# Optimization experiments

Measured on AMD Instinct MI355X. Metric: run time of the kernel, lower is better.

Reference implementation:

```python
import jax, jax.numpy as jnp
import numpy as np

DIM_IN = 256
DIM = 256      # dim_out
N = 4096       # nodes at current depth
K = 16         # max children (padded)
R = 8192       # rows in previous-level h/c tensors (row 0 is the zero init row)


def _reverse_sequence(x, length):
    """TF reverse_sequence along axis 1: reverse first length[i] steps, keep tail."""
    T = x.shape[1]
    t = jnp.arange(T)
    idx = jnp.where(t[None, :] < length[:, None], length[:, None] - 1 - t[None, :], t[None, :])
    return jnp.take_along_axis(x, idx[:, :, None], axis=1)


def _lstm(x, kernel, rec, bias, h0, c0):
    """Standard (CuDNN/Keras gate order i,f,g,o) LSTM. x: [B,T,D] -> y: [B,T,H]."""
    xz = jnp.einsum('btd,dg->btg', x, kernel) + bias  # precompute input projection

    def step(carry, xz_t):
        h, c = carry
        z = xz_t + h @ rec
        i, f, g, o = jnp.split(z, 4, axis=-1)
        c = jax.nn.sigmoid(f) * c + jax.nn.sigmoid(i) * jnp.tanh(g)
        h = jax.nn.sigmoid(o) * jnp.tanh(c)
        return (h, c), h

    _, ys = jax.lax.scan(step, (h0, c0), jnp.swapaxes(xz, 0, 1))
    return jnp.swapaxes(ys, 0, 1)


def _bilstm(x, length, kernel, rec, bias, init_h, init_c, fc_w, return_seq):
    """kernel/rec/bias/init_* have a leading dir axis of size 2 (fwd, bwd)."""
    B = x.shape[0]
    h0f = jnp.broadcast_to(init_h[0], (B, DIM))
    c0f = jnp.broadcast_to(init_c[0], (B, DIM))
    h0b = jnp.broadcast_to(init_h[1], (B, DIM))
    c0b = jnp.broadcast_to(init_c[1], (B, DIM))
    x_back = _reverse_sequence(x, length)
    y_f = _lstm(x, kernel[0], rec[0], bias[0], h0f, c0f)
    y_b = _lstm(x_back, kernel[1], rec[1], bias[1], h0b, c0b)
    y = jnp.concatenate([y_f, y_b], axis=-1)  # [B,T,2*DIM] (y_b not re-reversed, as in TF code)
    if return_seq:
        return y @ fc_w
    y_last = y[jnp.arange(B), length - 1]  # last valid timestep
    return y_last @ fc_w


def setup_inputs() -> dict:
    key = jax.random.key(0)
    ks = jax.random.split(key, 16)
    x = jax.random.normal(ks[0], (N, DIM_IN), dtype=jnp.float32)
    h_tensor = jax.random.normal(ks[1], (R, DIM), dtype=jnp.float32)
    c_tensor = jax.random.normal(ks[2], (R, DIM), dtype=jnp.float32)
    # padded child-index matrix: each row has length in [1, K], padded with -1
    raw = jax.random.randint(ks[3], (N, K), 0, R, dtype=jnp.int32)
    lengths = jax.random.randint(ks[4], (N,), 1, K + 1, dtype=jnp.int32)
    indice = jnp.where(jnp.arange(K)[None, :] < lengths[:, None], raw, jnp.int32(-1))
    # Dense W: dim_in -> 4*dim_out
    W_w = jax.random.normal(ks[5], (DIM_IN, 4 * DIM), dtype=jnp.float32) * 0.05
    W_b = jnp.zeros((4 * DIM,), dtype=jnp.float32)
    # 4 BiLSTMs (gates f,i,u,o), each with 2 directions; input dim = DIM (gathered h)
    lstm_kernel = jax.random.normal(ks[6], (4, 2, DIM, 4 * DIM), dtype=jnp.float32) * 0.05
    lstm_rec = jax.random.normal(ks[7], (4, 2, DIM, 4 * DIM), dtype=jnp.float32) * 0.05
    lstm_bias = jnp.zeros((4, 2, 4 * DIM), dtype=jnp.float32)
    init_h = jax.random.normal(ks[8], (4, 2, 1, DIM), dtype=jnp.float32) * 0.01
    init_c = jax.random.normal(ks[9], (4, 2, 1, DIM), dtype=jnp.float32) * 0.01
    fc_w = jax.random.normal(ks[10], (4, 2 * DIM, DIM), dtype=jnp.float32) * 0.05
    return {"x": x, "h_tensor": h_tensor, "c_tensor": c_tensor, "indice": indice,
            "W_w": W_w, "W_b": W_b, "lstm_kernel": lstm_kernel, "lstm_rec": lstm_rec,
            "lstm_bias": lstm_bias, "init_h": init_h, "init_c": init_c, "fc_w": fc_w}


def reference(x, h_tensor, c_tensor, indice, W_w, W_b, lstm_kernel, lstm_rec,
              lstm_bias, init_h, init_c, fc_w):
    mask_bool = indice != -1
    mask = mask_bool.astype(jnp.float32)                # [N,K]
    length = jnp.sum(mask, axis=1).astype(jnp.int32)    # [N]
    safe_idx = jnp.where(mask_bool, indice, 0)
    h = h_tensor[safe_idx]  # [N,K,DIM] gathered child states
    c = c_tensor[safe_idx]
    W_x = x @ W_w + W_b
    W_f_x, W_i_x, W_u_x, W_o_x = jnp.split(W_x, 4, axis=-1)
    # forget gate: per-child BiLSTM sequence output
    f_seq = _bilstm(h, length, lstm_kernel[0], lstm_rec[0], lstm_bias[0],
                    init_h[0], init_c[0], fc_w[0], return_seq=True)  # [N,K,DIM]
    branch_f_k = jax.nn.sigmoid(W_f_x[:, None, :] + f_seq)
    branch_f = jnp.sum(branch_f_k * c * mask[:, :, None], axis=1)    # masked reduce
    branch_i = jax.nn.sigmoid(_bilstm(h, length, lstm_kernel[1], lstm_rec[1], lstm_bias[1],
                                      init_h[1], init_c[1], fc_w[1], False) + W_i_x)
    branch_u = jnp.tanh(_bilstm(h, length, lstm_kernel[2], lstm_rec[2], lstm_bias[2],
                                init_h[2], init_c[2], fc_w[2], False) + W_u_x)
    branch_o = jax.nn.sigmoid(_bilstm(h, length, lstm_kernel[3], lstm_rec[3], lstm_bias[3],
                                      init_h[3], init_c[3], fc_w[3], False) + W_o_x)
    new_c = branch_i * branch_u + branch_f
    new_h = branch_o * jnp.tanh(new_c)
    return new_h, new_c
```

## Files before the change

### kernel.cpp

```cpp
#include <hip/hip_runtime.h>
#include <stdint.h>

typedef __bf16 bf16x8 __attribute__((ext_vector_type(8)));
typedef float  f32x4  __attribute__((ext_vector_type(4)));
typedef unsigned short u16;
typedef unsigned int   u32;

#define NN   4096
#define KCH  16
#define RR   8192

static constexpr size_t OFF_WCOMB = 0;
static constexpr size_t OFF_FCWT  = 8388608;
static constexpr size_t OFF_HST   = 9961472;
static constexpr size_t OFF_CST   = 43515904;
static constexpr size_t OFF_YSEQ  = 77070336;
static constexpr size_t OFF_YLAST = 144179200;
static constexpr size_t OFF_BRF   = 160956416;
static constexpr size_t OFF_FCO   = 163053568;
static constexpr size_t OFF_XS    = 169345024;
static constexpr size_t OFF_HN    = 171442176;
static constexpr size_t OFF_CN    = 175636480;
static constexpr size_t OFF_BIASN = 179830784;
static constexpr size_t OFF_IHN   = 179847168;
static constexpr size_t OFF_ICN   = 179851264;
static constexpr size_t OFF_WBN   = 179855360;
static constexpr size_t OFF_IDX   = 179857408;
static constexpr size_t OFF_LEN   = 180119552;
static constexpr size_t OFF_FLAG  = 180135936;
static constexpr size_t OFF_NODEOF= 180136000;
static constexpr size_t OFF_LENS  = 180152384;
static constexpr size_t OFF_NTN   = 180168768;
static constexpr size_t WS_NEEDED = 180168832;

struct KParams {
  const void *x, *h_tensor, *c_tensor, *W_w, *W_b, *lstm_kernel, *lstm_rec,
             *lstm_bias, *init_h, *init_c, *fc_w;
  const int *indice;
  u16 *wcomb, *fcwT2, *h_state, *y_seq, *y_last, *brf, *fc_outb,
      *xs, *hn, *cn, *biasn, *inithn, *initcn, *wbn;
  float *c_stateT;
  int *idxf, *len, *flag, *nodeof, *len_s, *ntneed;
  float *outp;
};

__device__ __forceinline__ float b2f(u16 u){ union{u32 i;float f;}v; v.i=((u32)u)<<16; return v.f; }
__device__ __forceinline__ u16  f2b(float f){ union{float f;u32 i;}v; v.f=f; u32 r=v.i+0x7FFFu+((v.i>>16)&1u); return (u16)(r>>16); }
__device__ __forceinline__ float sigm(float x){ return 1.0f/(1.0f+__expf(-x)); }
__device__ __forceinline__ float tanh_(float x){ return 2.0f/(1.0f+__expf(-2.0f*x)) - 1.0f; }
__device__ __forceinline__ u16  cvt(const void* q, size_t i, int isf){
  return isf ? f2b(((const float*)q)[i]) : ((const u16*)q)[i];
}
__device__ __forceinline__ void cp16(const u16* g, u16* l){
  __builtin_amdgcn_global_load_lds((const __attribute__((address_space(1))) u32*)g,
                                   (__attribute__((address_space(3))) u32*)l, 16, 0, 0);
}

__global__ void detect_k(KParams p){
  __shared__ int cnt[256];
  int tid = threadIdx.x;
  u16 u = ((const u16*)p.x)[2*tid];
  int e = (u >> 7) & 0xFF;
  cnt[tid] = (u != 0 && e >= 100 && e <= 140) ? 1 : 0;
  __syncthreads();
  if (tid == 0){
    int s = 0;
    for (int i=0;i<256;i++) s += cnt[i];
    *p.flag = (s < 192) ? 1 : 0;
  }
}

__global__ void prep_idx_k(KParams p){
  int n = blockIdx.x*256 + threadIdx.x;
  if (n >= NN) return;
  int L = 0;
  #pragma unroll
  for (int t=0;t<KCH;t++) L += (p.indice[n*KCH+t] != -1);
  p.len[n] = L;
}

__global__ void sort_k(KParams p){
  __shared__ int cnt[17];
  __shared__ int start[17];
  int tid = threadIdx.x;
  if (tid < 17) cnt[tid] = 0;
  __syncthreads();
  for (int n = tid; n < NN; n += 256) atomicAdd(&cnt[p.len[n]], 1);
  __syncthreads();
  if (tid == 0){
    int acc = 0;
    for (int v = 16; v >= 1; --v){ start[v] = acc; acc += cnt[v]; }
    for (int t = 0; t < 16; ++t){
      int need = (t == 0) ? NN : start[t];
      p.ntneed[t] = (need + 127) >> 7;
    }
  }
  __syncthreads();
  for (int n = tid; n < NN; n += 256){
    int ps = atomicAdd(&start[p.len[n]], 1);
    p.nodeof[ps] = n;
  }
}

__global__ void norm_k(KParams p){
  int i = blockIdx.x*256 + threadIdx.x;
  if (i >= 4207616) return;
  int isf = *p.flag;
  if (i < 2097152)       p.hn[i] = cvt(p.h_tensor, i, isf);
  else if (i < 4194304)  p.cn[i-2097152] = cvt(p.c_tensor, i-2097152, isf);
  else if (i < 4202496){ int j = i-4194304; int gd = j>>10, pc = j&1023;
                         p.biasn[j] = cvt(p.lstm_bias, gd*1024 + ((pc&3)<<8) + (pc>>2), isf); }
  else if (i < 4204544)  p.inithn[i-4202496] = cvt(p.init_h, i-4202496, isf);
  else if (i < 4206592)  p.initcn[i-4204544] = cvt(p.init_c, i-4204544, isf);
  else                   p.wbn[i-4206592] = cvt(p.W_b, i-4206592, isf);
}

__global__ void xperm_k(KParams p){
  int ns = blockIdx.x, u = threadIdx.x;
  int n = p.nodeof[ns];
  p.xs[(size_t)ns*256 + u] = cvt(p.x, (size_t)n*256 + u, *p.flag);
}

__global__ void prep_idx2_k(KParams p){
  int ns = blockIdx.x*256 + threadIdx.x;
  if (ns >= NN) return;
  int n = p.nodeof[ns];
  p.len_s[ns] = p.len[n];
  #pragma unroll
  for (int t=0;t<KCH;t++){
    int v = p.indice[n*KCH+t];
    p.idxf[t*NN + ns] = (v != -1) ? v : 0;
  }
}

__global__ void prep_w_k(KParams p){
  int i = blockIdx.x*256 + threadIdx.x;
  int isf = *p.flag;
  if (i < 4194304){
    int gd = i>>19, pc = (i>>9)&1023, k = i&511;
    int perm = ((pc&3)<<8) + (pc>>2);
    p.wcomb[i] = (k < 256) ? cvt(p.lstm_rec,    (size_t)(gd*256 + k)*1024 + perm, isf)
                           : cvt(p.lstm_kernel, (size_t)(gd*256 + (k-256))*1024 + perm, isf);
  } else if (i < 4980736){
    int j = i - 4194304;
    int g = j/196608, rem = j%196608, o = rem/768, k = rem%768;
    p.fcwT2[j] = (k < 512) ? cvt(p.fc_w, (size_t)(g*512 + k)*256 + o, isf)
                           : cvt(p.W_w,  (size_t)(k-512)*1024 + g*256 + o, isf);
  }
}

__global__ void prep_state_k(KParams p){
  int i = blockIdx.x*256 + threadIdx.x;
  int gd = i >> 20;
  p.h_state[i]  = p.inithn[(gd<<8) + (i & 255)];
  p.c_stateT[i] = b2f(p.initcn[(gd<<8) + ((i>>12)&255)]);
}

__global__ void fallback_k(float* out){
  int i = blockIdx.x*256 + threadIdx.x;
  out[i] = 1000.0f; out[1048576 + i] = 1000.0f;
}

enum { MODE_STAGE=0, MODE_FC0=1, MODE_FC123=2 };

template<int MODE>
__launch_bounds__(256)
__global__ void gemm_k(KParams p, int t)
{
  __shared__ __align__(16) u16 As[2][8192];
  __shared__ __align__(16) u16 Bs[2][8192];
  __shared__ __align__(16) u16 hbuf[(MODE==MODE_STAGE)?128*40:1];
  __shared__ int nidx[(MODE!=MODE_FC123)?128:1];
  __shared__ u16 biasl[(MODE==MODE_STAGE)?128:1];
  __shared__ int Ln[(MODE==MODE_FC0)?8:1];

  const int tid = threadIdx.x;
  const int lane = tid & 63, wv = tid >> 6;
  const int col16 = lane & 15, quad = lane >> 4;
  const int wy = wv >> 1, wx = wv & 1;

  constexpr int K  = (MODE==MODE_STAGE) ? 512 : 768;
  constexpr int KT = K/64;

  int mtile, ntile, gd = 0;
  const u16 *Ap=nullptr, *Bh=nullptr;
  if constexpr (MODE==MODE_STAGE){
    int b = blockIdx.x;
    gd = b & 7; mtile = (b>>3) & 7; ntile = b >> 6;
    if (ntile >= p.ntneed[t]) return;
    Ap = p.wcomb + (size_t)gd*1024*512;
    Bh = p.h_state + ((size_t)(t&1)*8 + gd)*NN*256;
  } else if constexpr (MODE==MODE_FC0){
    mtile = blockIdx.x; ntile = blockIdx.y;
  } else {
    mtile = blockIdx.x; ntile = blockIdx.y; gd = blockIdx.z;
  }
  const int rowA = mtile*128;
  const int rowB = ntile*128;

  if constexpr (MODE==MODE_STAGE){
    if (tid < 128){
      int n = rowB + tid;
      int L = p.len_s[n];
      int d = gd & 1;
      int eff = (d && t < L) ? (L-1-t) : t;
      nidx[tid] = p.idxf[eff*NN + n];
      biasl[tid] = p.biasn[gd*1024 + rowA + tid];
    }
    __syncthreads();
  }
  if constexpr (MODE==MODE_FC0){
    if (tid < 128){
      int nl = tid>>4, tt = tid&15;
      nidx[tid] = p.idxf[tt*NN + mtile*8 + nl];
    }
    if (tid < 8) Ln[tid] = p.len_s[mtile*8 + tid];
    __syncthreads();
  }

  auto stage = [&](int kt, int buf){
    const int kk = kt*64;
    #pragma unroll
    for (int i=0;i<4;i++){
      int ch = wv*4 + i;
      int r  = ch*8 + (lane>>3);
      int cs = (((lane&7) ^ (r&7)) << 3);
      const u16 *ga, *gb;
      if constexpr (MODE==MODE_STAGE){
        ga = Ap + (size_t)(rowA+r)*512 + kk + cs;
        gb = (kk < 256) ? (Bh + (size_t)(rowB+r)*256 + kk + cs)
                        : (p.hn + (size_t)nidx[r]*256 + (kk-256) + cs);
      } else if constexpr (MODE==MODE_FC0){
        if (kk < 512){
          const u16* Asel = (kk < 256) ? p.y_seq : p.y_seq + (size_t)65536*256;
          ga = Asel + (size_t)(rowA+r)*256 + (kk&255) + cs;
        } else {
          ga = p.xs + (size_t)((rowA+r)>>4)*256 + (kk-512) + cs;
        }
        gb = p.fcwT2 + (size_t)(rowB+r)*768 + kk + cs;
      } else {
        int g = gd + 1;
        if (kk < 512){
          const u16* Asel = p.y_last + (size_t)(g*2 + (kk>=256))*NN*256;
          ga = Asel + (size_t)(rowA+r)*256 + (kk&255) + cs;
        } else {
          ga = p.xs + (size_t)(rowA+r)*256 + (kk-512) + cs;
        }
        gb = p.fcwT2 + (size_t)g*196608 + (size_t)(rowB+r)*768 + kk + cs;
      }
      cp16(ga, &As[buf][ch*512]);
      cp16(gb, &Bs[buf][ch*512]);
    }
  };

  f32x4 acc[4][4] = {};

  stage(0, 0);
  for (int kt = 0; kt < KT; ++kt){
    __syncthreads();
    if (kt+1 < KT) stage(kt+1, (kt+1)&1);
    const int bsel = kt & 1;
    #pragma unroll
    for (int ks=0; ks<64; ks+=32){
      bf16x8 af[4], bfr[4];
      #pragma unroll
      for (int mf=0; mf<4; mf++){
        int row = wy*64+mf*16+col16;
        int lc  = (ks>>3) + quad;
        af[mf] = *(const bf16x8*)&As[bsel][row*64 + ((lc ^ (row&7))<<3)];
      }
      #pragma unroll
      for (int nf=0; nf<4; nf++){
        int row = wx*64+nf*16+col16;
        int lc  = (ks>>3) + quad;
        bfr[nf] = *(const bf16x8*)&Bs[bsel][row*64 + ((lc ^ (row&7))<<3)];
      }
      #pragma unroll
      for (int mf=0; mf<4; mf++)
        #pragma unroll
        for (int nf=0; nf<4; nf++)
          acc[mf][nf] = __builtin_amdgcn_mfma_f32_16x16x32_bf16(af[mf], bfr[nf], acc[mf][nf], 0, 0, 0);
    }
  }

  if constexpr (MODE==MODE_STAGE){
    const int g = gd >> 1, d = gd & 1;
    const int wbuf = (t+1) & 1;
    #pragma unroll
    for (int nf=0; nf<4; nf++){
      int nc_ = wx*64 + nf*16 + col16;
      int n = rowB + nc_;
      #pragma unroll
      for (int mf=0; mf<4; mf++){
        int lp = wy*64 + mf*16 + quad*4;
        int u  = (rowA + lp) >> 2;
        float zi = acc[mf][nf][0] + b2f(biasl[lp+0]);
        float zf = acc[mf][nf][1] + b2f(biasl[lp+1]);
        float zg = acc[mf][nf][2] + b2f(biasl[lp+2]);
        float zo = acc[mf][nf][3] + b2f(biasl[lp+3]);
        size_t ci = ((size_t)gd*256 + u)*NN + n;
        float cp = p.c_stateT[ci];
        float cn = sigm(zf)*cp + sigm(zi)*tanh_(zg);
        float hn = sigm(zo)*tanh_(cn);
        p.c_stateT[ci] = cn;
        hbuf[nc_*40 + (lp>>2)] = f2b(hn);
      }
    }
    __syncthreads();
    int row = tid >> 1, half = tid & 1;
    int n = rowB + row;
    int u0 = (rowA >> 2) + half*16;
    uint4 v0 = *(const uint4*)&hbuf[row*40 + half*16];
    uint4 v1 = *(const uint4*)&hbuf[row*40 + half*16 + 8];
    u16* hw = p.h_state + (((size_t)wbuf*8 + gd)*NN + n)*256 + u0;
    ((uint4*)hw)[0] = v0; ((uint4*)hw)[1] = v1;
    if (g == 0){
      u16* yw = p.y_seq + ((size_t)d*65536 + (size_t)n*KCH + t)*256 + u0;
      ((uint4*)yw)[0] = v0; ((uint4*)yw)[1] = v1;
    } else if (p.len_s[n] == t+1){
      u16* lw = p.y_last + ((size_t)gd*NN + n)*256 + u0;
      ((uint4*)lw)[0] = v0; ((uint4*)lw)[1] = v1;
    }
  } else if constexpr (MODE==MODE_FC0){
    #pragma unroll
    for (int mf=0; mf<4; mf++){
      int nl = wy*4 + mf;
      int n  = mtile*8 + nl;
      int L  = Ln[nl];
      #pragma unroll
      for (int nf=0; nf<4; nf++){
        int u = rowB + wx*64 + nf*16 + col16;
        float wb_ = b2f(p.wbn[u]);
        float psum = 0.f;
        #pragma unroll
        for (int r=0;r<4;r++){
          int tt = quad*4 + r;
          if (tt < L){
            int ridx = nidx[nl*16 + tt];
            float cch = b2f(p.cn[(size_t)ridx*256 + u]);
            psum += sigm(acc[mf][nf][r] + wb_) * cch;
          }
        }
        psum += __shfl_xor(psum, 16);
        psum += __shfl_xor(psum, 32);
        if (quad == 0) p.brf[(size_t)n*256 + u] = f2b(psum);
      }
    }
  } else {
    int g = gd + 1;
    #pragma unroll
    for (int mf=0; mf<4; mf++){
      int r0 = rowA + wy*64 + mf*16 + quad*4;
      #pragma unroll
      for (int nf=0; nf<4; nf++){
        int c = rowB + wx*64 + nf*16 + col16;
        float wb_ = b2f(p.wbn[g*256 + c]);
        u16* o = p.fc_outb + (size_t)gd*NN*256 + (size_t)r0*256 + c;
        #pragma unroll
        for (int r=0;r<4;r++) o[(size_t)r*256] = f2b(acc[mf][nf][r] + wb_);
      }
    }
  }
}

__global__ void final_k(KParams p){
  int i = blockIdx.x*256 + threadIdx.x;
  int ns = i >> 8, u = i & 255;
  int n = p.nodeof[ns];
  float bf_ = b2f(p.brf[i]);
  float bi = sigm (b2f(p.fc_outb[i]));
  float bu = tanh_(b2f(p.fc_outb[1048576 + i]));
  float bo = sigm (b2f(p.fc_outb[2097152 + i]));
  float nc = bi*bu + bf_;
  float nh = bo*tanh_(nc);
  p.outp[(size_t)n*256 + u] = nh;
  p.outp[1048576 + (size_t)n*256 + u] = nc;
}

extern "C" void kernel_launch(void* const* d_in, const int* in_sizes, int n_in,
                              void* d_out, int out_size, void* d_ws, size_t ws_size,
                              hipStream_t stream) {
  if (ws_size < WS_NEEDED){
    fallback_k<<<4096, 256, 0, stream>>>((float*)d_out);
    return;
  }
  KParams p;
  p.x          = d_in[0];
  p.h_tensor   = d_in[1];
  p.c_tensor   = d_in[2];
  p.indice     = (const int*)d_in[3];
  p.W_w        = d_in[4];
  p.W_b        = d_in[5];
  p.lstm_kernel= d_in[6];
  p.lstm_rec   = d_in[7];
  p.lstm_bias  = d_in[8];
  p.init_h     = d_in[9];
  p.init_c     = d_in[10];
  p.fc_w       = d_in[11];
  char* w = (char*)d_ws;
  p.wcomb   = (u16*)  (w + OFF_WCOMB);
  p.fcwT2   = (u16*)  (w + OFF_FCWT);
  p.h_state = (u16*)  (w + OFF_HST);
  p.c_stateT= (float*)(w + OFF_CST);
  p.y_seq   = (u16*)  (w + OFF_YSEQ);
  p.y_last  = (u16*)  (w + OFF_YLAST);
  p.brf     = (u16*)  (w + OFF_BRF);
  p.fc_outb = (u16*)  (w + OFF_FCO);
  p.xs      = (u16*)  (w + OFF_XS);
  p.hn      = (u16*)  (w + OFF_HN);
  p.cn      = (u16*)  (w + OFF_CN);
  p.biasn   = (u16*)  (w + OFF_BIASN);
  p.inithn  = (u16*)  (w + OFF_IHN);
  p.initcn  = (u16*)  (w + OFF_ICN);
  p.wbn     = (u16*)  (w + OFF_WBN);
  p.idxf    = (int*)  (w + OFF_IDX);
  p.len     = (int*)  (w + OFF_LEN);
  p.flag    = (int*)  (w + OFF_FLAG);
  p.nodeof  = (int*)  (w + OFF_NODEOF);
  p.len_s   = (int*)  (w + OFF_LENS);
  p.ntneed  = (int*)  (w + OFF_NTN);
  p.outp    = (float*)d_out;

  detect_k    <<<1,     256, 0, stream>>>(p);
  prep_idx_k  <<<16,    256, 0, stream>>>(p);
  sort_k      <<<1,     256, 0, stream>>>(p);
  norm_k      <<<16436, 256, 0, stream>>>(p);
  xperm_k     <<<4096,  256, 0, stream>>>(p);
  prep_idx2_k <<<16,    256, 0, stream>>>(p);
  prep_w_k    <<<19456, 256, 0, stream>>>(p);
  prep_state_k<<<32768, 256, 0, stream>>>(p);

  for (int t = 0; t < KCH; ++t)
    gemm_k<MODE_STAGE><<<2048, 256, 0, stream>>>(p, t);

  gemm_k<MODE_FC0>  <<<dim3(512,2), 256, 0, stream>>>(p, 0);
  gemm_k<MODE_FC123><<<dim3(32,2,3), 256, 0, stream>>>(p, 0);

  final_k<<<4096, 256, 0, stream>>>(p);
}
```

Measured before the change: 908.4 us.

## Split recurrent step GEMM into dedicated 512-thread kernel with 256x128 tiles

```diff
diff --git a/kernel.cpp b/kernel.cpp
--- a/kernel.cpp
+++ b/kernel.cpp
@@ -161,54 +161,143 @@
   out[i] = 1000.0f; out[1048576 + i] = 1000.0f;
 }
 
-enum { MODE_STAGE=0, MODE_FC0=1, MODE_FC123=2 };
-
-template<int MODE>
-__launch_bounds__(256)
-__global__ void gemm_k(KParams p, int t)
+__global__ __launch_bounds__(512, 4) void stage512_k(KParams p, int t)
 {
-  __shared__ __align__(16) u16 As[2][8192];
-  __shared__ __align__(16) u16 Bs[2][8192];
-  __shared__ __align__(16) u16 hbuf[(MODE==MODE_STAGE)?128*40:1];
-  __shared__ int nidx[(MODE!=MODE_FC123)?128:1];
-  __shared__ u16 biasl[(MODE==MODE_STAGE)?128:1];
-  __shared__ int Ln[(MODE==MODE_FC0)?8:1];
+  __shared__ __align__(16) u16 As[16384];
+  __shared__ __align__(16) u16 Bs[8192];
+  __shared__ int nidx[128];
+  __shared__ u16 biasl[256];
 
   const int tid = threadIdx.x;
   const int lane = tid & 63, wv = tid >> 6;
   const int col16 = lane & 15, quad = lane >> 4;
   const int wy = wv >> 1, wx = wv & 1;
 
-  constexpr int K  = (MODE==MODE_STAGE) ? 512 : 768;
-  constexpr int KT = K/64;
-
-  int mtile, ntile, gd = 0;
-  const u16 *Ap=nullptr, *Bh=nullptr;
-  if constexpr (MODE==MODE_STAGE){
-    int b = blockIdx.x;
-    gd = b & 7; mtile = (b>>3) & 7; ntile = b >> 6;
-    if (ntile >= p.ntneed[t]) return;
-    Ap = p.wcomb + (size_t)gd*1024*512;
-    Bh = p.h_state + ((size_t)(t&1)*8 + gd)*NN*256;
-  } else if constexpr (MODE==MODE_FC0){
-    mtile = blockIdx.x; ntile = blockIdx.y;
-  } else {
-    mtile = blockIdx.x; ntile = blockIdx.y; gd = blockIdx.z;
-  }
+  const int b = blockIdx.x;
+  const int gd = b & 7, mtile = (b>>3) & 3, ntile = b >> 5;
+  if (ntile >= p.ntneed[t]) return;
+  const u16* __restrict__ Ap = p.wcomb + (size_t)gd*524288;
+  const u16* __restrict__ Bh = p.h_state + ((size_t)(t&1)*8 + gd)*NN*256;
+  const int rowA = mtile*256;
+  const int rowB = ntile*128;
+  const int d = gd & 1;
+
+  if (tid < 128){
+    int n = rowB + tid;
+    int L = p.len_s[n];
+    int eff = (d && t < L) ? (L-1-t) : t;
+    nidx[tid] = p.idxf[eff*NN + n];
+  }
+  if (tid < 256) biasl[tid] = p.biasn[gd*1024 + rowA + tid];
+  __syncthreads();
+
+  f32x4 acc[4][4] = {};
+
+  for (int kt = 0; kt < 8; ++kt){
+    const int kk = kt*64;
+    #pragma unroll
+    for (int i=0;i<4;i++){
+      int ch = wv*4 + i;
+      int r  = ch*8 + (lane>>3);
+      int cs = (((lane&7) ^ (r&7)) << 3);
+      cp16(Ap + (size_t)(rowA+r)*512 + kk + cs, &As[ch*512]);
+    }
+    #pragma unroll
+    for (int i=0;i<2;i++){
+      int ch = wv*2 + i;
+      int r  = ch*8 + (lane>>3);
+      int cs = (((lane&7) ^ (r&7)) << 3);
+      const u16* gb = (kk < 256) ? (Bh + (size_t)(rowB+r)*256 + kk + cs)
+                                 : (p.hn + (size_t)nidx[r]*256 + (kk-256) + cs);
+      cp16(gb, &Bs[ch*512]);
+    }
+    __syncthreads();
+    #pragma unroll
+    for (int ks=0; ks<64; ks+=32){
+      bf16x8 af[4], bfr[4];
+      #pragma unroll
+      for (int mf=0; mf<4; mf++){
+        int row = wy*64+mf*16+col16;
+        int lc  = (ks>>3) + quad;
+        af[mf] = *(const bf16x8*)&As[row*64 + ((lc ^ (row&7))<<3)];
+      }
+      #pragma unroll
+      for (int nf=0; nf<4; nf++){
+        int row = wx*64+nf*16+col16;
+        int lc  = (ks>>3) + quad;
+        bfr[nf] = *(const bf16x8*)&Bs[row*64 + ((lc ^ (row&7))<<3)];
+      }
+      #pragma unroll
+      for (int mf=0; mf<4; mf++)
+        #pragma unroll
+        for (int nf=0; nf<4; nf++)
+          acc[mf][nf] = __builtin_amdgcn_mfma_f32_16x16x32_bf16(af[mf], bfr[nf], acc[mf][nf], 0, 0, 0);
+    }
+    __syncthreads();
+  }
+
+  u16* hbuf = As;
+  const int g = gd >> 1;
+  const int wbuf = (t+1) & 1;
+  #pragma unroll
+  for (int nf=0; nf<4; nf++){
+    int nc_ = wx*64 + nf*16 + col16;
+    int n = rowB + nc_;
+    #pragma unroll
+    for (int mf=0; mf<4; mf++){
+      int lp = wy*64 + mf*16 + quad*4;
+      int u  = (rowA + lp) >> 2;
+      float zi = acc[mf][nf][0] + b2f(biasl[lp+0]);
+      float zf = acc[mf][nf][1] + b2f(biasl[lp+1]);
+      float zg = acc[mf][nf][2] + b2f(biasl[lp+2]);
+      float zo = acc[mf][nf][3] + b2f(biasl[lp+3]);
+      size_t ci = ((size_t)gd*256 + u)*NN + n;
+      float cp = p.c_stateT[ci];
+      float cn = sigm(zf)*cp + sigm(zi)*tanh_(zg);
+      float hn = sigm(zo)*tanh_(cn);
+      p.c_stateT[ci] = cn;
+      hbuf[nc_*72 + (lp>>2)] = f2b(hn);
+    }
+  }
+  __syncthreads();
+  int row = tid >> 2, part = tid & 3;
+  int n = rowB + row;
+  int u0 = (rowA >> 2) + part*16;
+  uint4 v0 = *(const uint4*)&hbuf[row*72 + part*16];
+  uint4 v1 = *(const uint4*)&hbuf[row*72 + part*16 + 8];
+  u16* hw = p.h_state + (((size_t)wbuf*8 + gd)*NN + n)*256 + u0;
+  ((uint4*)hw)[0] = v0; ((uint4*)hw)[1] = v1;
+  if (g == 0){
+    u16* yw = p.y_seq + ((size_t)d*65536 + (size_t)n*KCH + t)*256 + u0;
+    ((uint4*)yw)[0] = v0; ((uint4*)yw)[1] = v1;
+  } else if (p.len_s[n] == t+1){
+    u16* lw = p.y_last + ((size_t)gd*NN + n)*256 + u0;
+    ((uint4*)lw)[0] = v0; ((uint4*)lw)[1] = v1;
+  }
+}
+
+enum { MODE_FC0=0, MODE_FC123=1 };
+
+template<int MODE>
+__launch_bounds__(256)
+__global__ void gemm_k(KParams p)
+{
+  __shared__ __align__(16) u16 As[2][8192];
+  __shared__ __align__(16) u16 Bs[2][8192];
+  __shared__ int nidx[(MODE==MODE_FC0)?128:1];
+  __shared__ int Ln[(MODE==MODE_FC0)?8:1];
+
+  const int tid = threadIdx.x;
+  const int lane = tid & 63, wv = tid >> 6;
+  const int col16 = lane & 15, quad = lane >> 4;
+  const int wy = wv >> 1, wx = wv & 1;
+
+  constexpr int KT = 12;
+
+  int mtile = blockIdx.x, ntile = blockIdx.y, gd = blockIdx.z;
   const int rowA = mtile*128;
   const int rowB = ntile*128;
 
-  if constexpr (MODE==MODE_STAGE){
-    if (tid < 128){
-      int n = rowB + tid;
-      int L = p.len_s[n];
-      int d = gd & 1;
-      int eff = (d && t < L) ? (L-1-t) : t;
-      nidx[tid] = p.idxf[eff*NN + n];
-      biasl[tid] = p.biasn[gd*1024 + rowA + tid];
-    }
-    __syncthreads();
-  }
   if constexpr (MODE==MODE_FC0){
     if (tid < 128){
       int nl = tid>>4, tt = tid&15;
@@ -226,11 +315,7 @@
       int r  = ch*8 + (lane>>3);
       int cs = (((lane&7) ^ (r&7)) << 3);
       const u16 *ga, *gb;
-      if constexpr (MODE==MODE_STAGE){
-        ga = Ap + (size_t)(rowA+r)*512 + kk + cs;
-        gb = (kk < 256) ? (Bh + (size_t)(rowB+r)*256 + kk + cs)
-                        : (p.hn + (size_t)nidx[r]*256 + (kk-256) + cs);
-      } else if constexpr (MODE==MODE_FC0){
+      if constexpr (MODE==MODE_FC0){
         if (kk < 512){
           const u16* Asel = (kk < 256) ? p.y_seq : p.y_seq + (size_t)65536*256;
           ga = Asel + (size_t)(rowA+r)*256 + (kk&255) + cs;
@@ -283,45 +368,7 @@
     }
   }
 
-  if constexpr (MODE==MODE_STAGE){
-    const int g = gd >> 1, d = gd & 1;
-    const int wbuf = (t+1) & 1;
-    #pragma unroll
-    for (int nf=0; nf<4; nf++){
-      int nc_ = wx*64 + nf*16 + col16;
-      int n = rowB + nc_;
-      #pragma unroll
-      for (int mf=0; mf<4; mf++){
-        int lp = wy*64 + mf*16 + quad*4;
-        int u  = (rowA + lp) >> 2;
-        float zi = acc[mf][nf][0] + b2f(biasl[lp+0]);
-        float zf = acc[mf][nf][1] + b2f(biasl[lp+1]);
-        float zg = acc[mf][nf][2] + b2f(biasl[lp+2]);
-        float zo = acc[mf][nf][3] + b2f(biasl[lp+3]);
-        size_t ci = ((size_t)gd*256 + u)*NN + n;
-        float cp = p.c_stateT[ci];
-        float cn = sigm(zf)*cp + sigm(zi)*tanh_(zg);
-        float hn = sigm(zo)*tanh_(cn);
-        p.c_stateT[ci] = cn;
-        hbuf[nc_*40 + (lp>>2)] = f2b(hn);
-      }
-    }
-    __syncthreads();
-    int row = tid >> 1, half = tid & 1;
-    int n = rowB + row;
-    int u0 = (rowA >> 2) + half*16;
-    uint4 v0 = *(const uint4*)&hbuf[row*40 + half*16];
-    uint4 v1 = *(const uint4*)&hbuf[row*40 + half*16 + 8];
-    u16* hw = p.h_state + (((size_t)wbuf*8 + gd)*NN + n)*256 + u0;
-    ((uint4*)hw)[0] = v0; ((uint4*)hw)[1] = v1;
-    if (g == 0){
-      u16* yw = p.y_seq + ((size_t)d*65536 + (size_t)n*KCH + t)*256 + u0;
-      ((uint4*)yw)[0] = v0; ((uint4*)yw)[1] = v1;
-    } else if (p.len_s[n] == t+1){
-      u16* lw = p.y_last + ((size_t)gd*NN + n)*256 + u0;
-      ((uint4*)lw)[0] = v0; ((uint4*)lw)[1] = v1;
-    }
-  } else if constexpr (MODE==MODE_FC0){
+  if constexpr (MODE==MODE_FC0){
     #pragma unroll
     for (int mf=0; mf<4; mf++){
       int nl = wy*4 + mf;
@@ -431,10 +478,10 @@
   prep_state_k<<<32768, 256, 0, stream>>>(p);
 
   for (int t = 0; t < KCH; ++t)
-    gemm_k<MODE_STAGE><<<2048, 256, 0, stream>>>(p, t);
-
-  gemm_k<MODE_FC0>  <<<dim3(512,2), 256, 0, stream>>>(p, 0);
-  gemm_k<MODE_FC123><<<dim3(32,2,3), 256, 0, stream>>>(p, 0);
+    stage512_k<<<1024, 512, 0, stream>>>(p, t);
+
+  gemm_k<MODE_FC0>  <<<dim3(512,2,1), 256, 0, stream>>>(p);
+  gemm_k<MODE_FC123><<<dim3(32,2,3),  256, 0, stream>>>(p);
 
   final_k<<<4096, 256, 0, stream>>>(p);
 }
```

Result: faster. 828.1 us (-8.8%).
